# Performance work log

Measured on AMD Instinct MI355X. Metric: run time of the kernel, lower is better.

The kernel has to match this reference:

```python
import jax, jax.numpy as jnp
import numpy as np
from jax import lax

B, T, NC = 256, 128, 96      # batch, MAX_SEQUENCE_LENGTH, NUM_CHORDS
H, LAT = 512, 512            # gru hidden, latent
CPB = 4                      # CHORDS_PER_BAR
NB = T // CPB                # bars
G = 3 * H                    # gru gate width


def _gru_cell(h, gx, Whh, bhh):
    # PyTorch GRU cell; gx = x @ Wih.T + bih precomputed. [B,3H]
    gh = h @ Whh.T + bhh
    r = jax.nn.sigmoid(gx[..., :H] + gh[..., :H])
    z = jax.nn.sigmoid(gx[..., H:2 * H] + gh[..., H:2 * H])
    n = jnp.tanh(gx[..., 2 * H:] + r * gh[..., 2 * H:])
    return (1.0 - z) * n + z * h


def _gru_layer(x, h0, Wih, Whh, bih, bhh):
    # x: [B,Tl,Din] -> ys [B,Tl,H], hT [B,H]
    gx = jnp.einsum('btd,gd->tbg', x, Wih) + bih
    def step(h, g):
        hn = _gru_cell(h, g, Whh, bhh)
        return hn, hn
    hT, ys = lax.scan(step, h0, gx)
    return ys.transpose(1, 0, 2), hT


def _bigru_layer(x, Wih, Whh, bih, bhh):
    h0 = jnp.zeros((x.shape[0], H), x.dtype)
    yf, hf = _gru_layer(x, h0, Wih[0], Whh[0], bih[0], bhh[0])
    yb, hb = _gru_layer(x[:, ::-1], h0, Wih[1], Whh[1], bih[1], bhh[1])
    return jnp.concatenate([yf, yb[:, ::-1]], -1), hf, hb


def setup_inputs():
    key = jax.random.key(0)
    it = iter(jax.random.split(key, 48))
    def p(*shape):
        return 0.05 * jax.random.normal(next(it), shape, jnp.float32)
    return {
        'input_chord_seqs': jax.random.uniform(next(it), (B, T, NC), jnp.float32),
        'length': jnp.full((B,), T, jnp.int32),
        'eps': jax.random.normal(next(it), (B, LAT), jnp.float32),
        'enc0_Wih': p(2, G, NC), 'enc0_Whh': p(2, G, H), 'enc0_bih': p(2, G), 'enc0_bhh': p(2, G),
        'enc1_Wih': p(2, G, 2 * H), 'enc1_Whh': p(2, G, H), 'enc1_bih': p(2, G), 'enc1_bhh': p(2, G),
        'con0_Wih': p(G, NC), 'con0_Whh': p(G, H), 'con0_bih': p(G), 'con0_bhh': p(G),
        'con1_Wih': p(G, H), 'con1_Whh': p(G, H), 'con1_bih': p(G), 'con1_bhh': p(G),
        'dec0_Wih': p(G, H + NC), 'dec0_Whh': p(G, H), 'dec0_bih': p(G), 'dec0_bhh': p(G),
        'dec1_Wih': p(G, H), 'dec1_Whh': p(G, H), 'dec1_bih': p(G), 'dec1_bhh': p(G),
        'W_mu': p(LAT, 4 * H), 'b_mu': p(LAT), 'W_lv': p(LAT, 4 * H), 'b_lv': p(LAT),
        'W_ci': p(NC, LAT), 'b_ci': p(NC),
        'W_ch': p(H, LAT), 'b_ch': p(H),
        'W_out': p(NC, H), 'b_out': p(NC),
    }


def _forward(input_chord_seqs, eps,
             enc0_Wih, enc0_Whh, enc0_bih, enc0_bhh,
             enc1_Wih, enc1_Whh, enc1_bih, enc1_bhh,
             con0_Wih, con0_Whh, con0_bih, con0_bhh,
             con1_Wih, con1_Whh, con1_bih, con1_bhh,
             dec0_Wih, dec0_Whh, dec0_bih, dec0_bhh,
             dec1_Wih, dec1_Whh, dec1_bih, dec1_bhh,
             W_mu, b_mu, W_lv, b_lv, W_ci, b_ci, W_ch, b_ch, W_out, b_out):
    # ---- encode (2-layer bidirectional GRU, full-length sequences) ----
    y0, h0f, h0b = _bigru_layer(input_chord_seqs, enc0_Wih, enc0_Whh, enc0_bih, enc0_bhh)
    _, h1f, h1b = _bigru_layer(y0, enc1_Wih, enc1_Whh, enc1_bih, enc1_bhh)
    # torch hidden layout (layers*dirs, B, H) -> transpose/view == [l0f,l0b,l1f,l1b]
    hidden = jnp.concatenate([h0f, h0b, h1f, h1b], -1)  # [B, 4H]
    mu = hidden @ W_mu.T + b_mu
    log_var = hidden @ W_lv.T + b_lv
    z = eps * jnp.exp(0.5 * log_var) + mu
    # ---- decode (teacher forcing path, eps_i=1) ----
    ci = z @ W_ci.T + b_ci                 # conductor input, constant across bars
    ch = z @ W_ch.T + b_ch                 # conductor h0, repeated for both layers
    gx_c0 = ci @ con0_Wih.T + con0_bih     # [B,3H] precomputed conductor l0 input proj
    bars = input_chord_seqs.reshape(B, NB, CPB, NC).transpose(1, 0, 2, 3)  # [NB,B,CPB,NC]
    def bar(carry, chb):
        h0c, h1c = carry
        h0c = _gru_cell(h0c, gx_c0, con0_Whh, con0_bhh)
        h1c = _gru_cell(h1c, h0c @ con1_Wih.T + con1_bih, con1_Whh, con1_bhh)
        emb = jnp.broadcast_to(h1c[:, None, :], (B, CPB, H))   # conductor embedding
        dec_in = jnp.concatenate([emb, chb], -1)               # [B,CPB,H+NC]
        d0, _ = _gru_layer(dec_in, h0c, dec0_Wih, dec0_Whh, dec0_bih, dec0_bhh)
        d1, _ = _gru_layer(d0, h1c, dec1_Wih, dec1_Whh, dec1_bih, dec1_bhh)
        return (h0c, h1c), d1 @ W_out.T + b_out
    _, chords = lax.scan(bar, (ch, ch), bars)                  # [NB,B,CPB,NC]
    logits = chords.transpose(1, 0, 2, 3).reshape(B, T, NC)
    return logits, mu, log_var


def reference(input_chord_seqs, length, eps,
              enc0_Wih, enc0_Whh, enc0_bih, enc0_bhh,
              enc1_Wih, enc1_Whh, enc1_bih, enc1_bhh,
              con0_Wih, con0_Whh, con0_bih, con0_bhh,
              con1_Wih, con1_Whh, con1_bih, con1_bhh,
              dec0_Wih, dec0_Whh, dec0_bih, dec0_bhh,
              dec1_Wih, dec1_Whh, dec1_bih, dec1_bhh,
              W_mu, b_mu, W_lv, b_lv, W_ci, b_ci, W_ch, b_ch, W_out, b_out):
    # length is all-T (full sequences), so packing is a no-op
    logits, mu, log_var = _forward(
        input_chord_seqs, eps,
        enc0_Wih, enc0_Whh, enc0_bih, enc0_bhh,
        enc1_Wih, enc1_Whh, enc1_bih, enc1_bhh,
        con0_Wih, con0_Whh, con0_bih, con0_bhh,
        con1_Wih, con1_Whh, con1_bih, con1_bhh,
        dec0_Wih, dec0_Whh, dec0_bih, dec0_bhh,
        dec1_Wih, dec1_Whh, dec1_bih, dec1_bhh,
        W_mu, b_mu, W_lv, b_lv, W_ci, b_ci, W_ch, b_ch, W_out, b_out)
    return (jax.nn.softmax(logits, -1), jax.nn.log_softmax(logits, -1), mu, log_var, input_chord_seqs)
```

## Files before the change

kernel.cpp:

```cpp
#include <hip/hip_runtime.h>


#define BB   256
#define TT   128
#define NCC  96
#define HDIM 512
#define GG   1536
#define NBB  32
#define CPBB 4

typedef __attribute__((ext_vector_type(4))) float f32x4;
typedef __attribute__((ext_vector_type(8))) short bf16x8;
typedef unsigned short ushort_t;

__device__ __forceinline__ unsigned short f2b(float x) {
  unsigned int u = __builtin_bit_cast(unsigned int, x);
  u += 0x7fff + ((u >> 16) & 1);
  return (unsigned short)(u >> 16);
}
__device__ __forceinline__ float b2f(unsigned short h) {
  unsigned int u = ((unsigned int)h) << 16;
  return __builtin_bit_cast(float, u);
}
__device__ __forceinline__ uint2 packA(float4 v) {
  uint2 r;
  r.x = (unsigned)f2b(v.x) | ((unsigned)f2b(v.y) << 16);
  r.y = (unsigned)f2b(v.z) | ((unsigned)f2b(v.w) << 16);
  return r;
}
__device__ __forceinline__ uint4 packA8(float4 v0, float4 v1) {
  uint4 r;
  r.x = (unsigned)f2b(v0.x) | ((unsigned)f2b(v0.y) << 16);
  r.y = (unsigned)f2b(v0.z) | ((unsigned)f2b(v0.w) << 16);
  r.z = (unsigned)f2b(v1.x) | ((unsigned)f2b(v1.y) << 16);
  r.w = (unsigned)f2b(v1.z) | ((unsigned)f2b(v1.w) << 16);
  return r;
}

struct CvtAll {
  const float* s[11];
  ushort_t* d[11];
  int n4[11];
};
__global__ void cvt_all_k(CvtAll a) {
  int e = blockIdx.z;
  int i = blockIdx.x * 256 + threadIdx.x;
  if (i >= a.n4[e]) return;
  float4 v = reinterpret_cast<const float4*>(a.s[e])[i];
  ushort4 o;
  o.x = f2b(v.x); o.y = f2b(v.y); o.z = f2b(v.z); o.w = f2b(v.w);
  reinterpret_cast<ushort4*>(a.d[e])[i] = o;
}

struct GruP {
  const float* h_prev; int hs; int hz;
  const ushort_t* Whh;
  const float* x0f; const ushort_t* x0b; int x0s;
  const ushort_t* W0; int w0ld; int K0;
  const float* x1f; int x1sp; const ushort_t* W1; int w1ld; int K1;
  const float* gxf;
  const ushort_t* gxb; int gxros;
  const float* bih; const float* bhh;
  float* h_out; int os;
  ushort_t* h_out2; int o2s;
};
struct GruP2 { GruP d[2]; };

#define LB3(WP, WLD_, G_, KOFF) \
  (*reinterpret_cast<const uint2*>((WP) + (size_t)((G_) * HDIM + c0 + bn) * (size_t)(WLD_) + (KOFF) + bk))

#define AL_H(KOFF, DST)  DST = packA(*reinterpret_cast<const float4*>(p.h_prev + (size_t)(r0 + arow) * p.hs + (KOFF) + ak));
#define AL_X0F(KOFF, DST) DST = packA(*reinterpret_cast<const float4*>(p.x0f + (size_t)(r0 + arow) * p.x0s + (KOFF) + ak));
#define AL_X0B(KOFF, DST) DST = *reinterpret_cast<const uint2*>(p.x0b + (size_t)(r0 + arow) * p.x0s + (KOFF) + ak);
#define AL_CH(KOFF, DST) { int rr_ = r0 + arow; \
  DST = packA(*reinterpret_cast<const float4*>(p.x1f + (size_t)(rr_ & 255) * 12288 + (rr_ >> 8) * 384 + p.x1sp * 96 + (KOFF) + ak)); }

#define GRU_MMA(B_, ACCN)                                                      \
  { bf16x8 afr = *reinterpret_cast<const bf16x8*>(&Xs[B_][wr * 16 + (lane & 15)][(lane >> 4) * 8]); \
    bf16x8 f0 = *reinterpret_cast<const bf16x8*>(&Bs[B_][0][wc * 16 + (lane & 15)][(lane >> 4) * 8]); \
    bf16x8 f1 = *reinterpret_cast<const bf16x8*>(&Bs[B_][1][wc * 16 + (lane & 15)][(lane >> 4) * 8]); \
    bf16x8 f2 = *reinterpret_cast<const bf16x8*>(&Bs[B_][2][wc * 16 + (lane & 15)][(lane >> 4) * 8]); \
    aR = __builtin_amdgcn_mfma_f32_16x16x32_bf16(afr, f0, aR, 0, 0, 0);        \
    aZ = __builtin_amdgcn_mfma_f32_16x16x32_bf16(afr, f1, aZ, 0, 0, 0);        \
    ACCN = __builtin_amdgcn_mfma_f32_16x16x32_bf16(afr, f2, ACCN, 0, 0, 0); }

#define GRU_PHASE(KLEN, ALOAD, WP, WLD_, ACCN)                                 \
  { uint2 aP0, aP1;                                                            \
    uint2 b0P0, b1P0, b2P0, b0P1, b1P1, b2P1;                                  \
    ALOAD(0, aP0)                                                              \
    b0P0 = LB3(WP, WLD_, 0, 0); b1P0 = LB3(WP, WLD_, 1, 0); b2P0 = LB3(WP, WLD_, 2, 0); \
    if ((KLEN) > 32) {                                                         \
      ALOAD(32, aP1)                                                           \
      b0P1 = LB3(WP, WLD_, 0, 32); b1P1 = LB3(WP, WLD_, 1, 32); b2P1 = LB3(WP, WLD_, 2, 32); \
    }                                                                          \
    __syncthreads();                                                           \
    for (int k0 = 0; k0 < (KLEN); k0 += 64) {                                  \
      *reinterpret_cast<uint2*>(&Xs[0][arow][ak]) = aP0;                       \
      *reinterpret_cast<uint2*>(&Bs[0][0][bn][bk]) = b0P0;                     \
      *reinterpret_cast<uint2*>(&Bs[0][1][bn][bk]) = b1P0;                     \
      *reinterpret_cast<uint2*>(&Bs[0][2][bn][bk]) = b2P0;                     \
      if (k0 + 64 < (KLEN)) {                                                  \
        ALOAD(k0 + 64, aP0)                                                    \
        b0P0 = LB3(WP, WLD_, 0, k0 + 64); b1P0 = LB3(WP, WLD_, 1, k0 + 64); b2P0 = LB3(WP, WLD_, 2, k0 + 64); \
      }                                                                        \
      __syncthreads();                                                         \
      GRU_MMA(0, ACCN)                                                         \
      if (k0 + 32 < (KLEN)) {                                                  \
        *reinterpret_cast<uint2*>(&Xs[1][arow][ak]) = aP1;                     \
        *reinterpret_cast<uint2*>(&Bs[1][0][bn][bk]) = b0P1;                   \
        *reinterpret_cast<uint2*>(&Bs[1][1][bn][bk]) = b1P1;                   \
        *reinterpret_cast<uint2*>(&Bs[1][2][bn][bk]) = b2P1;                   \
        if (k0 + 96 < (KLEN)) {                                                \
          ALOAD(k0 + 96, aP1)                                                  \
          b0P1 = LB3(WP, WLD_, 0, k0 + 96); b1P1 = LB3(WP, WLD_, 1, k0 + 96); b2P1 = LB3(WP, WLD_, 2, k0 + 96); \
        }                                                                      \
        __syncthreads();                                                       \
        GRU_MMA(1, ACCN)                                                       \
      }                                                                        \
    } }

__global__ __launch_bounds__(256) void gru_k(GruP2 pp)
{
  const GruP p = pp.d[blockIdx.z];
  __shared__ ushort_t Xs[2][32][40];
  __shared__ ushort_t Bs[2][3][32][40];
  const int tid = threadIdx.x;
  const int lane = tid & 63, wv = tid >> 6;
  const int wr = wv >> 1, wc = wv & 1;
  const int r0 = blockIdx.x * 32, c0 = blockIdx.y * 32;
  const int arow = tid >> 3, ak = (tid & 7) * 4;
  const int bn = tid >> 3, bk = (tid & 7) * 4;
  f32x4 aR = {}, aZ = {}, aNX = {}, aNH = {};

  if (!p.hz) { GRU_PHASE(HDIM, AL_H, p.Whh, HDIM, aNH) }
  if (p.K0 > 0) {
    if (p.x0b) { GRU_PHASE(p.K0, AL_X0B, p.W0, p.w0ld, aNX) }
    else       { GRU_PHASE(p.K0, AL_X0F, p.W0, p.w0ld, aNX) }
  }
  if (p.K1 > 0) { GRU_PHASE(p.K1, AL_CH, p.W1, p.w1ld, aNX) }

#pragma unroll
  for (int rg = 0; rg < 4; ++rg) {
    int r = r0 + wr * 16 + ((lane >> 4) << 2) + rg;
    int c = c0 + wc * 16 + (lane & 15);
    float sr = aR[rg] + p.bhh[c];
    float sz = aZ[rg] + p.bhh[HDIM + c];
    float nx = aNX[rg];
    float nh = aNH[rg] + p.bhh[2 * HDIM + c];
    if (p.bih) { sr += p.bih[c]; sz += p.bih[HDIM + c]; nx += p.bih[2 * HDIM + c]; }
    if (p.gxf) {
      const float* g = p.gxf + (size_t)r * GG;
      sr += g[c]; sz += g[HDIM + c]; nx += g[2 * HDIM + c];
    }
    if (p.gxb) {
      const ushort_t* g = p.gxb + (size_t)(p.gxros + r) * 1536;
      sr += b2f(g[c]); sz += b2f(g[HDIM + c]); nx += b2f(g[2 * HDIM + c]);
    }
    float rgate = 1.f / (1.f + expf(-sr));
    float zgate = 1.f / (1.f + expf(-sz));
    float ngate = tanhf(nx + rgate * nh);
    float hp = p.hz ? 0.f : p.h_prev[(size_t)r * p.hs + c];
    float hv = (1.f - zgate) * ngate + zgate * hp;
    p.h_out[(size_t)r * p.os + c] = hv;
    if (p.h_out2) p.h_out2[(size_t)r * p.o2s + c] = f2b(hv);
  }
}

__global__ __launch_bounds__(512) void gx_gemm_k(
    const ushort_t* __restrict__ Aarg, const ushort_t* __restrict__ W,
    int ldw, int dirWStride,
    const float* __restrict__ bias, ushort_t* __restrict__ C, int t0, int K)
{
  __shared__ ushort_t As[64][40];
  __shared__ ushort_t Bs[128][40];
  const int tid = threadIdx.x;
  const int lane = tid & 63, wv = tid >> 6;
  const int wr = wv >> 2, wc = wv & 3;
  const int rBase = blockIdx.x * 64, n0 = blockIdx.y * 128;
  const int dir = rBase >> 12;
  const int arow = tid >> 3, ak = (tid & 7) * 4;
  const int bcol = tid >> 2, bk = (tid & 3) * 8;
  int r = rBase + arow;
  int tl = (r >> 8) & 15, b = r & 255;
  int tsrc = (dir == 0) ? (t0 + tl) : (127 - t0 - tl);
  const ushort_t* apB = Aarg + (size_t)b * 131072 + (size_t)tsrc * 1024;
  const ushort_t* wrow = W + (size_t)dir * dirWStride + (size_t)(n0 + bcol) * ldw;
  f32x4 acc[2][2] = {};

  uint2 aC = *reinterpret_cast<const uint2*>(apB + ak);
  uint4 bC = *reinterpret_cast<const uint4*>(wrow + bk);
  for (int k0 = 0; k0 < K; k0 += 32) {
    __syncthreads();
    *reinterpret_cast<uint2*>(&As[arow][ak]) = aC;
    *reinterpret_cast<uint4*>(&Bs[bcol][bk]) = bC;
    if (k0 + 32 < K) {
      aC = *reinterpret_cast<const uint2*>(apB + k0 + 32 + ak);
      bC = *reinterpret_cast<const uint4*>(wrow + k0 + 32 + bk);
    }
    __syncthreads();
    bf16x8 af[2], bf[2];
#pragma unroll
    for (int i = 0; i < 2; ++i)
      af[i] = *reinterpret_cast<const bf16x8*>(&As[wr * 32 + i * 16 + (lane & 15)][(lane >> 4) * 8]);
#pragma unroll
    for (int j = 0; j < 2; ++j)
      bf[j] = *reinterpret_cast<const bf16x8*>(&Bs[wc * 32 + j * 16 + (lane & 15)][(lane >> 4) * 8]);
#pragma unroll
    for (int i = 0; i < 2; ++i)
#pragma unroll
      for (int j = 0; j < 2; ++j)
        acc[i][j] = __builtin_amdgcn_mfma_f32_16x16x32_bf16(af[i], bf[j], acc[i][j], 0, 0, 0);
  }
#pragma unroll
  for (int i = 0; i < 2; ++i)
#pragma unroll
    for (int j = 0; j < 2; ++j)
#pragma unroll
      for (int rg = 0; rg < 4; ++rg) {
        int rr = rBase + wr * 32 + i * 16 + ((lane >> 4) << 2) + rg;
        int cc = n0 + wc * 32 + j * 16 + (lane & 15);
        C[(size_t)rr * 1536 + cc] = f2b(acc[i][j][rg] + bias[dir * 1536 + cc]);
      }
}

__global__ __launch_bounds__(256) void gemm_demb_k(
    const float* __restrict__ A,
    const ushort_t* __restrict__ W, int ldw,
    const float* __restrict__ bias,
    ushort_t* __restrict__ C)
{
  __shared__ ushort_t As[32][40];
  __shared__ ushort_t Bs[64][40];
  const int tid = threadIdx.x;
  const int lane = tid & 63, wv = tid >> 6;
  const int wr = wv >> 1, wc = wv & 1;
  const int r0 = blockIdx.x * 32, c0 = blockIdx.y * 64;
  const int arow = tid >> 3, ak = (tid & 7) * 4;
  const int bn = tid >> 2, bk = (tid & 3) * 8;
  f32x4 acc[2] = {};
  const float* arowp = A + (size_t)(r0 + arow) * 512;
  const ushort_t* wrow = W + (size_t)(c0 + bn) * ldw;

  uint2 aC = packA(*reinterpret_cast<const float4*>(arowp + ak));
  uint4 bC = *reinterpret_cast<const uint4*>(wrow + bk);
  for (int k0 = 0; k0 < 512; k0 += 32) {
    __syncthreads();
    *reinterpret_cast<uint2*>(&As[arow][ak]) = aC;
    *reinterpret_cast<uint4*>(&Bs[bn][bk]) = bC;
    if (k0 + 32 < 512) {
      aC = packA(*reinterpret_cast<const float4*>(arowp + k0 + 32 + ak));
      bC = *reinterpret_cast<const uint4*>(wrow + k0 + 32 + bk);
    }
    __syncthreads();
    bf16x8 afr = *reinterpret_cast<const bf16x8*>(&As[wr * 16 + (lane & 15)][(lane >> 4) * 8]);
#pragma unroll
    for (int j = 0; j < 2; ++j) {
      bf16x8 bfr = *reinterpret_cast<const bf16x8*>(&Bs[wc * 32 + j * 16 + (lane & 15)][(lane >> 4) * 8]);
      acc[j] = __builtin_amdgcn_mfma_f32_16x16x32_bf16(afr, bfr, acc[j], 0, 0, 0);
    }
  }
#pragma unroll
  for (int j = 0; j < 2; ++j)
#pragma unroll
    for (int rg = 0; rg < 4; ++rg) {
      int r = r0 + wr * 16 + ((lane >> 4) << 2) + rg;
      int c = c0 + wc * 32 + j * 16 + (lane & 15);
      C[(size_t)r * 1536 + c] = f2b(acc[j][rg] + bias[c]);
    }
}

__global__ __launch_bounds__(256) void mfma_gemm_k(
    const float* __restrict__ A, int lda,
    const float* __restrict__ W, int ldw,
    const float* __restrict__ bias,
    float* __restrict__ C, int ldc, int N, int K)
{
  __shared__ ushort_t As[32][40];
  __shared__ ushort_t Bs[64][40];
  const int tid = threadIdx.x;
  const int lane = tid & 63, wv = tid >> 6;
  const int wr = wv >> 1, wc = wv & 1;
  const int r0 = blockIdx.x * 32, c0 = blockIdx.y * 64;
  const int arow = tid >> 3, ak = (tid & 7) * 4;
  const int bn = tid >> 2, bk = (tid & 3) * 8;
  f32x4 acc[2] = {};
  const int nOk = (c0 + bn) < N;
  const float* wrow = W + (size_t)(nOk ? (c0 + bn) : 0) * ldw;

  uint2 aC = packA(*reinterpret_cast<const float4*>(A + (size_t)(r0 + arow) * lda + ak));
  uint4 bC;
  {
    float4 v0 = *reinterpret_cast<const float4*>(wrow + bk);
    float4 v1 = *reinterpret_cast<const float4*>(wrow + bk + 4);
    bC = packA8(v0, v1);
  }
  for (int k0 = 0; k0 < K; k0 += 32) {
    __syncthreads();
    *reinterpret_cast<uint2*>(&As[arow][ak]) = aC;
    if (nOk) *reinterpret_cast<uint4*>(&Bs[bn][bk]) = bC;
    else { uint4 z; z.x = z.y = z.z = z.w = 0; *reinterpret_cast<uint4*>(&Bs[bn][bk]) = z; }
    if (k0 + 32 < K) {
      aC = packA(*reinterpret_cast<const float4*>(A + (size_t)(r0 + arow) * lda + k0 + 32 + ak));
      float4 v0 = *reinterpret_cast<const float4*>(wrow + k0 + 32 + bk);
      float4 v1 = *reinterpret_cast<const float4*>(wrow + k0 + 32 + bk + 4);
      bC = packA8(v0, v1);
    }
    __syncthreads();
    bf16x8 afr = *reinterpret_cast<const bf16x8*>(&As[wr * 16 + (lane & 15)][(lane >> 4) * 8]);
#pragma unroll
    for (int j = 0; j < 2; ++j) {
      bf16x8 bfr = *reinterpret_cast<const bf16x8*>(&Bs[wc * 32 + j * 16 + (lane & 15)][(lane >> 4) * 8]);
      acc[j] = __builtin_amdgcn_mfma_f32_16x16x32_bf16(afr, bfr, acc[j], 0, 0, 0);
    }
  }
#pragma unroll
  for (int j = 0; j < 2; ++j)
#pragma unroll
    for (int rg = 0; rg < 4; ++rg) {
      int r = r0 + wr * 16 + ((lane >> 4) << 2) + rg;
      int c = c0 + wc * 32 + j * 16 + (lane & 15);
      if (c < N) C[(size_t)r * ldc + c] = acc[j][rg] + (bias ? bias[c] : 0.f);
    }
}

__global__ void gather_hidden_k(const ushort_t* __restrict__ y0b,
                                const float* __restrict__ h1f,
                                const float* __restrict__ h1b,
                                float* __restrict__ hidden)
{
  int i = blockIdx.x * 256 + threadIdx.x;
  if (i >= BB * 4 * HDIM) return;
  int b = i >> 11, j = i & 2047;
  float v;
  if (j < 512)       v = b2f(y0b[(size_t)b * 131072 + 127 * 1024 + j]);
  else if (j < 1024) v = b2f(y0b[(size_t)b * 131072 + j]);
  else if (j < 1536) v = h1f[b * 512 + (j - 1024)];
  else               v = h1b[b * 512 + (j - 1536)];
  hidden[i] = v;
}

__global__ void z_k(const float* __restrict__ mu, const float* __restrict__ lv,
                    const float* __restrict__ eps, float* __restrict__ z,
                    float* __restrict__ out_mu, float* __restrict__ out_lv)
{
  int i = blockIdx.x * 256 + threadIdx.x;
  if (i >= BB * HDIM) return;
  float m = mu[i], l = lv[i];
  z[i] = eps[i] * expf(0.5f * l) + m;
  out_mu[i] = m;
  out_lv[i] = l;
}

__global__ void softmax_k(const float* __restrict__ logits,
                          float* __restrict__ out_sm,
                          float* __restrict__ out_lsm)
{
  int q = blockIdx.x;
  int lane = threadIdx.x;
  const float* row = logits + (size_t)q * 96;
  float v0 = row[lane];
  float v1 = (lane < 32) ? row[lane + 64] : -1e30f;
  float m = fmaxf(v0, v1);
#pragma unroll
  for (int o = 32; o; o >>= 1) m = fmaxf(m, __shfl_xor(m, o));
  float e0 = expf(v0 - m);
  float e1 = (lane < 32) ? expf(v1 - m) : 0.f;
  float s = e0 + e1;
#pragma unroll
  for (int o = 32; o; o >>= 1) s += __shfl_xor(s, o);
  float inv = 1.f / s, ls = logf(s);
  int b = (q >> 2) & 255;
  int t = (q >> 10) * 4 + (q & 3);
  size_t base = (size_t)b * TT * 96 + (size_t)t * 96;
  out_sm[base + lane]  = e0 * inv;
  out_lsm[base + lane] = v0 - m - ls;
  if (lane < 32) {
    out_sm[base + lane + 64]  = e1 * inv;
    out_lsm[base + lane + 64] = v1 - m - ls;
  }
}

__global__ void echo_k(const float* __restrict__ in, float* __restrict__ out)
{
  int i = blockIdx.x * 256 + threadIdx.x;
  if (i < BB * TT * NCC) out[i] = in[i];
}

extern "C" void kernel_launch(void* const* d_in, const int* in_sizes, int n_in,
                              void* d_out, int out_size, void* d_ws, size_t ws_size,
                              hipStream_t stream)
{
  const float* in        = (const float*)d_in[0];
  const float* eps       = (const float*)d_in[2];
  const float* enc0_Wih  = (const float*)d_in[3];
  const float* enc0_Whh  = (const float*)d_in[4];
  const float* enc0_bih  = (const float*)d_in[5];
  const float* enc0_bhh  = (const float*)d_in[6];
  const float* enc1_Wih  = (const float*)d_in[7];
  const float* enc1_Whh  = (const float*)d_in[8];
  const float* enc1_bih  = (const float*)d_in[9];
  const float* enc1_bhh  = (const float*)d_in[10];
  const float* con0_Wih  = (const float*)d_in[11];
  const float* con0_Whh  = (const float*)d_in[12];
  const float* con0_bih  = (const float*)d_in[13];
  const float* con0_bhh  = (const float*)d_in[14];
  const float* con1_Wih  = (const float*)d_in[15];
  const float* con1_Whh  = (const float*)d_in[16];
  const float* con1_bih  = (const float*)d_in[17];
  const float* con1_bhh  = (const float*)d_in[18];
  const float* dec0_Wih  = (const float*)d_in[19];
  const float* dec0_Whh  = (const float*)d_in[20];
  const float* dec0_bih  = (const float*)d_in[21];
  const float* dec0_bhh  = (const float*)d_in[22];
  const float* dec1_Wih  = (const float*)d_in[23];
  const float* dec1_Whh  = (const float*)d_in[24];
  const float* dec1_bih  = (const float*)d_in[25];
  const float* dec1_bhh  = (const float*)d_in[26];
  const float* W_mu      = (const float*)d_in[27];
  const float* b_mu      = (const float*)d_in[28];
  const float* W_lv      = (const float*)d_in[29];
  const float* b_lv      = (const float*)d_in[30];
  const float* W_ci      = (const float*)d_in[31];
  const float* b_ci      = (const float*)d_in[32];
  const float* W_ch      = (const float*)d_in[33];
  const float* b_ch      = (const float*)d_in[34];
  const float* W_out     = (const float*)d_in[35];
  const float* b_out     = (const float*)d_in[36];

  float* ws = (float*)d_ws;
  ushort_t* y0b  = (ushort_t*)ws;
  float* e0pp    = ws + 16777216;
  ushort_t* gxAll = (ushort_t*)(ws + 17301504);
  float* h0c   = ws;
  float* h1c   = ws + 4194304;
  float* d0p[2] = { ws + 8388608,  ws + 12582912 };
  float* d1p[2] = { ws + 16777216, ws + 20971520 };
  float* mu_f  = ws + 26492928;
  float* lv_f  = ws + 26624000;
  float* zz    = ws + 26755072;
  float* ci    = ws + 26886144;
  float* chv   = ws + 26910720;
  float* gx_c0 = ws + 27041792;
  ushort_t* Wb = (ushort_t*)(ws + 27435008);

  ushort_t* wb_e0_Wih = Wb;
  ushort_t* wb_e0_Whh = Wb + 294912;
  ushort_t* wb_e1_Wih = Wb + 1867776;
  ushort_t* wb_e1_Whh = Wb + 5013504;
  ushort_t* wb_c0_Whh = Wb + 6586368;
  ushort_t* wb_c1_Wih = Wb + 7372800;
  ushort_t* wb_c1_Whh = Wb + 8159232;
  ushort_t* wb_d0_Wih = Wb + 8945664;
  ushort_t* wb_d0_Whh = Wb + 9879552;
  ushort_t* wb_d1_Wih = Wb + 10665984;
  ushort_t* wb_d1_Whh = Wb + 11452416;

  float* outp   = (float*)d_out;
  float* out_sm = outp;
  float* out_ls = outp + 3145728;
  float* out_mu = outp + 6291456;
  float* out_lv = outp + 6422528;
  float* out_ec = outp + 6553600;
  ushort_t* gx_demb = (ushort_t*)outp;
  float* fscr = out_ec;
  float* h1f_pp[2] = { fscr,          fscr + 131072 };
  float* h1b_pp[2] = { fscr + 262144, fscr + 393216 };
  float* hidden    = fscr + 524288;
  float* logits_q  = out_ec;

  auto gemmM = [&](const float* A, int lda, const float* W, int ldw, const float* bias,
                   float* C, int ldc, int M, int N, int K) {
    mfma_gemm_k<<<dim3(M / 32, (N + 63) / 64), 256, 0, stream>>>(A, lda, W, ldw, bias, C, ldc, N, K);
  };
  auto gru2 = [&](const GruP& a, const GruP& b, int rows) {
    GruP2 q; q.d[0] = a; q.d[1] = b;
    gru_k<<<dim3(rows / 32, 16, 2), 256, 0, stream>>>(q);
  };
  auto gru1 = [&](const GruP& a, int rows) {
    GruP2 q; q.d[0] = a; q.d[1] = a;
    gru_k<<<dim3(rows / 32, 16, 1), 256, 0, stream>>>(q);
  };

  {
    CvtAll ca;
    const float* srcs[11] = { enc0_Wih, enc0_Whh, enc1_Wih, enc1_Whh, con0_Whh,
                              con1_Wih, con1_Whh, dec0_Wih, dec0_Whh, dec1_Wih, dec1_Whh };
    ushort_t* dsts[11] = { wb_e0_Wih, wb_e0_Whh, wb_e1_Wih, wb_e1_Whh, wb_c0_Whh,
                           wb_c1_Wih, wb_c1_Whh, wb_d0_Wih, wb_d0_Whh, wb_d1_Wih, wb_d1_Whh };
    int ns[11] = { 294912, 1572864, 3145728, 1572864, 786432,
                   786432, 786432, 933888, 786432, 786432, 786432 };
    for (int e = 0; e < 11; ++e) { ca.s[e] = srcs[e]; ca.d[e] = dsts[e]; ca.n4[e] = ns[e] / 4; }
    cvt_all_k<<<dim3(3072, 1, 11), 256, 0, stream>>>(ca);
  }

  for (int t = 0; t < TT; ++t) {
    int tr = TT - 1 - t;
    GruP f = {};
    f.hz = (t == 0);
    f.h_prev = e0pp + (size_t)((t + 1) & 1) * 262144; f.hs = 512;
    f.x0f = in + (size_t)t * 96; f.x0s = 12288; f.W0 = wb_e0_Wih; f.w0ld = 96; f.K0 = 96;
    f.Whh = wb_e0_Whh; f.bih = enc0_bih; f.bhh = enc0_bhh;
    f.h_out = e0pp + (size_t)(t & 1) * 262144; f.os = 512;
    f.h_out2 = y0b + (size_t)t * 1024; f.o2s = 131072;
    GruP bd = {};
    bd.hz = (t == 0);
    bd.h_prev = e0pp + (size_t)((t + 1) & 1) * 262144 + 131072; bd.hs = 512;
    bd.x0f = in + (size_t)tr * 96; bd.x0s = 12288;
    bd.W0 = wb_e0_Wih + 147456; bd.w0ld = 96; bd.K0 = 96;
    bd.Whh = wb_e0_Whh + 786432; bd.bih = enc0_bih + GG; bd.bhh = enc0_bhh + GG;
    bd.h_out = e0pp + (size_t)(t & 1) * 262144 + 131072; bd.os = 512;
    bd.h_out2 = y0b + (size_t)tr * 1024 + 512; bd.o2s = 131072;
    gru2(f, bd, BB);
  }

  for (int ch = 0; ch < 8; ++ch) {
    int t0 = ch * 16;
    gx_gemm_k<<<dim3(128, 12), 512, 0, stream>>>(
        y0b, wb_e1_Wih, 1024, 1572864, enc1_bih, gxAll, t0, 1024);
    for (int tl = 0; tl < 16; ++tl) {
      int t = t0 + tl;
      GruP f = {};
      f.hz = (t == 0);
      f.h_prev = h1f_pp[(t + 1) & 1]; f.hs = 512;
      f.Whh = wb_e1_Whh; f.bhh = enc1_bhh;
      f.gxb = gxAll; f.gxros = tl * 256;
      f.h_out = h1f_pp[t & 1]; f.os = 512;
      GruP bd = {};
      bd.hz = (t == 0);
      bd.h_prev = h1b_pp[(t + 1) & 1]; bd.hs = 512;
      bd.Whh = wb_e1_Whh + 786432; bd.bhh = enc1_bhh + GG;
      bd.gxb = gxAll + 6291456; bd.gxros = tl * 256;
      bd.h_out = h1b_pp[t & 1]; bd.os = 512;
      gru2(f, bd, BB);
    }
  }

  gather_hidden_k<<<2048, 256, 0, stream>>>(y0b, h1f_pp[1], h1b_pp[1], hidden);
  gemmM(hidden, 2048, W_mu, 2048, b_mu, mu_f, 512, BB, 512, 2048);
  gemmM(hidden, 2048, W_lv, 2048, b_lv, lv_f, 512, BB, 512, 2048);
  z_k<<<512, 256, 0, stream>>>(mu_f, lv_f, eps, zz, out_mu, out_lv);
  gemmM(zz, 512, W_ci, 512, b_ci, ci, 96, BB, 96, 512);
  gemmM(zz, 512, W_ch, 512, b_ch, chv, 512, BB, 512, 512);
  gemmM(ci, 96, con0_Wih, 96, con0_bih, gx_c0, GG, BB, GG, 96);

  auto c0desc = [&](int bar) {
    GruP c0 = {};
    c0.h_prev = (bar == 0) ? chv : h0c + (size_t)(bar - 1) * 131072; c0.hs = 512;
    c0.gxf = gx_c0;
    c0.Whh = wb_c0_Whh; c0.bhh = con0_bhh;
    c0.h_out = h0c + (size_t)bar * 131072; c0.os = 512;
    return c0;
  };
  auto c1desc = [&](int bar) {
    GruP c1 = {};
    c1.h_prev = (bar == 0) ? chv : h1c + (size_t)(bar - 1) * 131072; c1.hs = 512;
    c1.x0f = h0c + (size_t)bar * 131072; c1.x0s = 512;
    c1.W0 = wb_c1_Wih; c1.w0ld = 512; c1.K0 = 512;
    c1.Whh = wb_c1_Whh; c1.bih = con1_bih; c1.bhh = con1_bhh;
    c1.h_out = h1c + (size_t)bar * 131072; c1.os = 512;
    return c1;
  };
  gru1(c0desc(0), BB);
  for (int bar = 1; bar < NBB; ++bar) gru2(c0desc(bar), c1desc(bar - 1), BB);
  gru1(c1desc(NBB - 1), BB);

  gemm_demb_k<<<dim3(256, 24), 256, 0, stream>>>(h1c, wb_d0_Wih, 608, dec0_bih, gx_demb);
  const int R = NBB * BB;
  for (int s = 0; s < CPBB; ++s) {
    GruP d0 = {};
    d0.h_prev = (s == 0) ? h0c : d0p[(s - 1) & 1]; d0.hs = 512;
    d0.x1f = in; d0.x1sp = s; d0.W1 = wb_d0_Wih + 512; d0.w1ld = 608; d0.K1 = 96;
    d0.gxb = gx_demb; d0.gxros = 0;
    d0.Whh = wb_d0_Whh; d0.bhh = dec0_bhh;
    d0.h_out = d0p[s & 1]; d0.os = 512;
    gru1(d0, R);
    GruP d1 = {};
    d1.h_prev = (s == 0) ? h1c : d1p[(s - 1) & 1]; d1.hs = 512;
    d1.x0f = d0p[s & 1]; d1.x0s = 512; d1.W0 = wb_d1_Wih; d1.w0ld = 512; d1.K0 = 512;
    d1.Whh = wb_d1_Whh; d1.bih = dec1_bih; d1.bhh = dec1_bhh;
    d1.h_out = d1p[s & 1]; d1.os = 512;
    gru1(d1, R);
    gemmM(d1p[s & 1], 512, W_out, 512, b_out, logits_q + (size_t)s * 96, 384, R, 96, 512);
  }

  softmax_k<<<NBB * BB * CPBB, 64, 0, stream>>>(logits_q, out_sm, out_ls);
  echo_k<<<12288, 256, 0, stream>>>(in, out_ec);
}
```

Before: 4.365 ms.

## Add split-K register-direct GRU step kernel for latency-bound recurrent launches

Result: slower. 5.710 ms (+30.8%).

```diff
diff --git a/kernel.cpp b/kernel.cpp
--- a/kernel.cpp
+++ b/kernel.cpp
@@ -35,6 +35,9 @@
   r.z = (unsigned)f2b(v1.x) | ((unsigned)f2b(v1.y) << 16);
   r.w = (unsigned)f2b(v1.z) | ((unsigned)f2b(v1.w) << 16);
   return r;
+}
+__device__ __forceinline__ bf16x8 packA8v(float4 v0, float4 v1) {
+  return __builtin_bit_cast(bf16x8, packA8(v0, v1));
 }
 
 struct CvtAll {
@@ -66,6 +69,133 @@
 };
 struct GruP2 { GruP d[2]; };
 
+#define MFMA_ __builtin_amdgcn_mfma_f32_16x16x32_bf16
+
+__device__ __forceinline__ void ldfragL(
+    const GruP& p, int ci, int nH, int nX0,
+    int arowg, int sl, int colg,
+    bf16x8& a, bf16x8& w0, bf16x8& w1, bf16x8& w2, int& isH)
+{
+  if (ci < nH) {
+    int ko = ci * 32 + sl;
+    const float* ap = p.h_prev + (size_t)arowg * p.hs + ko;
+    a = packA8v(*reinterpret_cast<const float4*>(ap),
+                *reinterpret_cast<const float4*>(ap + 4));
+    const ushort_t* w = p.Whh + (size_t)colg * 512 + ko;
+    w0 = *reinterpret_cast<const bf16x8*>(w);
+    w1 = *reinterpret_cast<const bf16x8*>(w + 262144);
+    w2 = *reinterpret_cast<const bf16x8*>(w + 524288);
+    isH = 1;
+  } else if (ci < nH + nX0) {
+    int ko = (ci - nH) * 32 + sl;
+    if (p.x0b) {
+      a = *reinterpret_cast<const bf16x8*>(p.x0b + (size_t)arowg * p.x0s + ko);
+    } else {
+      const float* ap = p.x0f + (size_t)arowg * p.x0s + ko;
+      a = packA8v(*reinterpret_cast<const float4*>(ap),
+                  *reinterpret_cast<const float4*>(ap + 4));
+    }
+    const ushort_t* w = p.W0 + (size_t)colg * p.w0ld + ko;
+    w0 = *reinterpret_cast<const bf16x8*>(w);
+    w1 = *reinterpret_cast<const bf16x8*>(w + (size_t)512 * p.w0ld);
+    w2 = *reinterpret_cast<const bf16x8*>(w + (size_t)1024 * p.w0ld);
+    isH = 0;
+  } else {
+    int ko = (ci - nH - nX0) * 32 + sl;
+    const float* ap = p.x1f + (size_t)(arowg & 255) * 12288 + (arowg >> 8) * 384
+                      + p.x1sp * 96 + ko;
+    a = packA8v(*reinterpret_cast<const float4*>(ap),
+                *reinterpret_cast<const float4*>(ap + 4));
+    const ushort_t* w = p.W1 + (size_t)colg * p.w1ld + ko;
+    w0 = *reinterpret_cast<const bf16x8*>(w);
+    w1 = *reinterpret_cast<const bf16x8*>(w + (size_t)512 * p.w1ld);
+    w2 = *reinterpret_cast<const bf16x8*>(w + (size_t)1024 * p.w1ld);
+    isH = 0;
+  }
+}
+
+__global__ __launch_bounds__(256) void gruL_k(GruP2 pp)
+{
+  const GruP p = pp.d[blockIdx.z];
+  __shared__ float red[2][64][17];
+  const int tid = threadIdx.x;
+  const int lane = tid & 63, wv = tid >> 6;
+  const int wr = wv & 1, kh = wv >> 1;
+  const int r0 = blockIdx.x * 32, c0 = blockIdx.y * 16;
+  const int sl = (lane >> 4) * 8;
+  const int arowg = r0 + wr * 16 + (lane & 15);
+  const int colg = c0 + (lane & 15);
+  f32x4 aR = {}, aZ = {}, aNX = {}, aNH = {};
+
+  const int nH = p.hz ? 0 : 16;
+  const int nX0 = p.K0 >> 5;
+  const int nX1 = p.K1 >> 5;
+  const int nc = nH + nX0 + nX1;
+  const int nh2 = (nc + 1) >> 1;
+  const int base = kh ? nh2 : 0;
+  const int myn = kh ? (nc - nh2) : nh2;
+
+  bf16x8 a0, w00, w10, w20; int h0 = 0;
+  bf16x8 a1, w01, w11, w21; int h1 = 0;
+  if (0 < myn) ldfragL(p, base + 0, nH, nX0, arowg, sl, colg, a0, w00, w10, w20, h0);
+  if (1 < myn) ldfragL(p, base + 1, nH, nX0, arowg, sl, colg, a1, w01, w11, w21, h1);
+
+  for (int i = 0; i < myn; i += 2) {
+    {
+      aR = MFMA_(a0, w00, aR, 0, 0, 0);
+      aZ = MFMA_(a0, w10, aZ, 0, 0, 0);
+      if (h0) aNH = MFMA_(a0, w20, aNH, 0, 0, 0);
+      else    aNX = MFMA_(a0, w20, aNX, 0, 0, 0);
+    }
+    if (i + 2 < myn) ldfragL(p, base + i + 2, nH, nX0, arowg, sl, colg, a0, w00, w10, w20, h0);
+    if (i + 1 < myn) {
+      aR = MFMA_(a1, w01, aR, 0, 0, 0);
+      aZ = MFMA_(a1, w11, aZ, 0, 0, 0);
+      if (h1) aNH = MFMA_(a1, w21, aNH, 0, 0, 0);
+      else    aNX = MFMA_(a1, w21, aNX, 0, 0, 0);
+    }
+    if (i + 3 < myn) ldfragL(p, base + i + 3, nH, nX0, arowg, sl, colg, a1, w01, w11, w21, h1);
+  }
+
+  if (kh == 1) {
+#pragma unroll
+    for (int rg = 0; rg < 4; ++rg) {
+      red[wr][lane][rg]      = aR[rg];
+      red[wr][lane][4 + rg]  = aZ[rg];
+      red[wr][lane][8 + rg]  = aNX[rg];
+      red[wr][lane][12 + rg] = aNH[rg];
+    }
+  }
+  __syncthreads();
+  if (kh == 0) {
+#pragma unroll
+    for (int rg = 0; rg < 4; ++rg) {
+      int r = r0 + wr * 16 + ((lane >> 4) << 2) + rg;
+      int c = c0 + (lane & 15);
+      float sr = aR[rg] + red[wr][lane][rg] + p.bhh[c];
+      float sz = aZ[rg] + red[wr][lane][4 + rg] + p.bhh[HDIM + c];
+      float nx = aNX[rg] + red[wr][lane][8 + rg];
+      float nh = aNH[rg] + red[wr][lane][12 + rg] + p.bhh[2 * HDIM + c];
+      if (p.bih) { sr += p.bih[c]; sz += p.bih[HDIM + c]; nx += p.bih[2 * HDIM + c]; }
+      if (p.gxf) {
+        const float* g = p.gxf + (size_t)r * GG;
+        sr += g[c]; sz += g[HDIM + c]; nx += g[2 * HDIM + c];
+      }
+      if (p.gxb) {
+        const ushort_t* g = p.gxb + (size_t)(p.gxros + r) * 1536;
+        sr += b2f(g[c]); sz += b2f(g[HDIM + c]); nx += b2f(g[2 * HDIM + c]);
+      }
+      float rgate = 1.f / (1.f + expf(-sr));
+      float zgate = 1.f / (1.f + expf(-sz));
+      float ngate = tanhf(nx + rgate * nh);
+      float hp = p.hz ? 0.f : p.h_prev[(size_t)r * p.hs + c];
+      float hv = (1.f - zgate) * ngate + zgate * hp;
+      p.h_out[(size_t)r * p.os + c] = hv;
+      if (p.h_out2) p.h_out2[(size_t)r * p.o2s + c] = f2b(hv);
+    }
+  }
+}
+
 #define LB3(WP, WLD_, G_, KOFF) \
   (*reinterpret_cast<const uint2*>((WP) + (size_t)((G_) * HDIM + c0 + bn) * (size_t)(WLD_) + (KOFF) + bk))
 
@@ -80,9 +210,9 @@
     bf16x8 f0 = *reinterpret_cast<const bf16x8*>(&Bs[B_][0][wc * 16 + (lane & 15)][(lane >> 4) * 8]); \
     bf16x8 f1 = *reinterpret_cast<const bf16x8*>(&Bs[B_][1][wc * 16 + (lane & 15)][(lane >> 4) * 8]); \
     bf16x8 f2 = *reinterpret_cast<const bf16x8*>(&Bs[B_][2][wc * 16 + (lane & 15)][(lane >> 4) * 8]); \
-    aR = __builtin_amdgcn_mfma_f32_16x16x32_bf16(afr, f0, aR, 0, 0, 0);        \
-    aZ = __builtin_amdgcn_mfma_f32_16x16x32_bf16(afr, f1, aZ, 0, 0, 0);        \
-    ACCN = __builtin_amdgcn_mfma_f32_16x16x32_bf16(afr, f2, ACCN, 0, 0, 0); }
+    aR = MFMA_(afr, f0, aR, 0, 0, 0);                                          \
+    aZ = MFMA_(afr, f1, aZ, 0, 0, 0);                                          \
+    ACCN = MFMA_(afr, f2, ACCN, 0, 0, 0); }
 
 #define GRU_PHASE(KLEN, ALOAD, WP, WLD_, ACCN)                                 \
   { uint2 aP0, aP1;                                                            \
@@ -472,9 +602,13 @@
                    float* C, int ldc, int M, int N, int K) {
     mfma_gemm_k<<<dim3(M / 32, (N + 63) / 64), 256, 0, stream>>>(A, lda, W, ldw, bias, C, ldc, N, K);
   };
-  auto gru2 = [&](const GruP& a, const GruP& b, int rows) {
+  auto gruL2 = [&](const GruP& a, const GruP& b) {
     GruP2 q; q.d[0] = a; q.d[1] = b;
-    gru_k<<<dim3(rows / 32, 16, 2), 256, 0, stream>>>(q);
+    gruL_k<<<dim3(8, 32, 2), 256, 0, stream>>>(q);
+  };
+  auto gruL1 = [&](const GruP& a) {
+    GruP2 q; q.d[0] = a; q.d[1] = a;
+    gruL_k<<<dim3(8, 32, 1), 256, 0, stream>>>(q);
   };
   auto gru1 = [&](const GruP& a, int rows) {
     GruP2 q; q.d[0] = a; q.d[1] = a;
@@ -510,7 +644,7 @@
     bd.Whh = wb_e0_Whh + 786432; bd.bih = enc0_bih + GG; bd.bhh = enc0_bhh + GG;
     bd.h_out = e0pp + (size_t)(t & 1) * 262144 + 131072; bd.os = 512;
     bd.h_out2 = y0b + (size_t)tr * 1024 + 512; bd.o2s = 131072;
-    gru2(f, bd, BB);
+    gruL2(f, bd);
   }
 
   for (int ch = 0; ch < 8; ++ch) {
@@ -531,7 +665,7 @@
       bd.Whh = wb_e1_Whh + 786432; bd.bhh = enc1_bhh + GG;
       bd.gxb = gxAll + 6291456; bd.gxros = tl * 256;
       bd.h_out = h1b_pp[t & 1]; bd.os = 512;
-      gru2(f, bd, BB);
+      gruL2(f, bd);
     }
   }
 
@@ -560,9 +694,9 @@
     c1.h_out = h1c + (size_t)bar * 131072; c1.os = 512;
     return c1;
   };
-  gru1(c0desc(0), BB);
-  for (int bar = 1; bar < NBB; ++bar) gru2(c0desc(bar), c1desc(bar - 1), BB);
-  gru1(c1desc(NBB - 1), BB);
+  gruL1(c0desc(0));
+  for (int bar = 1; bar < NBB; ++bar) gruL2(c0desc(bar), c1desc(bar - 1));
+  gruL1(c1desc(NBB - 1));
 
   gemm_demb_k<<<dim3(256, 24), 256, 0, stream>>>(h1c, wb_d0_Wih, 608, dec0_bih, gx_demb);
   const int R = NBB * BB;
```
